# Performance work log

Measured on AMD Instinct MI355X. Metric: run time of the kernel, lower is better.

The kernel has to match this reference:

```python
import jax, jax.numpy as jnp
import numpy as np

SAMPLE_RATE = 44100.0


def _peaking_coeffs(freq, gain_db, q, fs):
    """RBJ cookbook peaking-EQ biquad coefficients (as in dasp-pytorch).
    freq/gain_db/q: [B, K]. Returns normalized b0,b1,b2,a1,a2 each [B, K]."""
    A = jnp.power(10.0, gain_db / 40.0)
    w0 = 2.0 * jnp.pi * freq / fs
    cosw = jnp.cos(w0)
    alpha = jnp.sin(w0) / (2.0 * q)
    b0 = 1.0 + alpha * A
    b1 = -2.0 * cosw
    b2 = 1.0 - alpha * A
    a0 = 1.0 + alpha / A
    a1 = -2.0 * cosw
    a2 = 1.0 - alpha / A
    inv_a0 = 1.0 / a0
    return b0 * inv_a0, b1 * inv_a0, b2 * inv_a0, a1 * inv_a0, a2 * inv_a0


def setup_inputs() -> dict:
    key = jax.random.key(0)
    k1, k2, k3, k4 = jax.random.split(key, 4)
    B, C, T, K = 32, 2, 262144, 6
    audio = jax.random.normal(k1, (B, C, T), dtype=jnp.float32) * 0.1
    # realistic EQ parameter ranges
    frequencies = 100.0 + jax.random.uniform(k2, (B, K), dtype=jnp.float32) * 9900.0  # 100 Hz .. 10 kHz
    gains = jax.random.normal(k3, (B, K), dtype=jnp.float32) * 6.0                     # ~ +/- 6 dB
    q_factors = 0.5 + jax.random.uniform(k4, (B, K), dtype=jnp.float32) * 3.0          # 0.5 .. 3.5
    return {"audio": audio, "frequencies": frequencies, "gains": gains, "q_factors": q_factors}


def reference(audio, frequencies, gains, q_factors):
    # audio: [B, C, T]; per-batch cascade of K peaking biquads over time.
    B, C, T = audio.shape
    K = frequencies.shape[1]
    b0, b1, b2, a1, a2 = _peaking_coeffs(frequencies, gains, q_factors, SAMPLE_RATE)
    # [K, B, 1] for broadcasting over channels
    b0, b1, b2, a1, a2 = (jnp.transpose(c)[:, :, None] for c in (b0, b1, b2, a1, a2))

    def step(carry, x):  # x: [B, C], one time sample through the whole cascade
        s1, s2 = carry  # each [K, B, C], direct-form II transposed states
        y = x
        ns1, ns2 = [], []
        for k in range(K):  # small fixed band loop (structurally sequential cascade)
            yk = b0[k] * y + s1[k]
            ns1.append(b1[k] * y - a1[k] * yk + s2[k])
            ns2.append(b2[k] * y - a2[k] * yk)
            y = yk
        return (jnp.stack(ns1), jnp.stack(ns2)), y

    init = (jnp.zeros((K, B, C), audio.dtype), jnp.zeros((K, B, C), audio.dtype))
    xs = jnp.moveaxis(audio, 2, 0)  # [T, B, C]
    _, ys = jax.lax.scan(step, init, xs)
    return jnp.moveaxis(ys, 0, 2)  # [B, C, T]
```

## Files before the change

### kernel.cpp

```cpp
#include <hip/hip_runtime.h>
#include <math.h>

namespace {
constexpr int B = 32, C = 2, T = 262144, K = 6;
constexpr int SEG = 1024;
constexpr int L = T / SEG;
constexpr int NBC = B * C;
constexpr int NST = 2 * K;
constexpr int LOG2L = 8;
constexpr int GP = SEG / 64;
constexpr int LOG2GP = 4;
constexpr int TS = 16;
constexpr int NT = L / TS;
constexpr int WPB = SEG / 64;
constexpr float FS = 44100.0f;
}

__device__ __forceinline__ float rl(float v, int lane) {
  return __int_as_float(__builtin_amdgcn_readlane(__float_as_int(v), lane));
}

__global__ void eq_coeffs(const float* __restrict__ fr, const float* __restrict__ gn,
                          const float* __restrict__ qf, float* __restrict__ cf) {
  int i = blockIdx.x * blockDim.x + threadIdx.x;
  if (i >= B * K) return;
  float f = fr[i], g = gn[i], Q = qf[i];
  float A  = powf(10.0f, g * (1.0f / 40.0f));
  float w0 = 6.283185307179586f * f / FS;
  float cw = cosf(w0);
  float al = sinf(w0) / (2.0f * Q);
  float b0 = 1.0f + al * A;
  float b1 = -2.0f * cw;
  float b2 = 1.0f - al * A;
  float a0 = 1.0f + al / A;
  float a2 = 1.0f - al / A;
  float ia = 1.0f / a0;
  float* p = cf + i * 5;
  p[0] = b0 * ia; p[1] = b1 * ia; p[2] = b2 * ia; p[3] = b1 * ia; p[4] = a2 * ia;
}

template <bool WRITE_OUT>
__global__ __launch_bounds__(64, 1) void eq_pass(const float* __restrict__ x,
                                                 const float* __restrict__ cf,
                                                 const float* __restrict__ st_in,
                                                 float* __restrict__ st_out,
                                                 float* __restrict__ y) {
  __shared__ float sIn[2][64][17];
  __shared__ float sOut[2][64][17];

  int l = threadIdx.x;
  int wid = blockIdx.x;
  int bc = wid / WPB;
  int segbase = (wid % WPB) * 64;
  int b = bc / C;
  int tid = bc * SEG + segbase + l;

  float b0[K], b1[K], b2[K], a1[K], a2[K];
#pragma unroll
  for (int k = 0; k < K; ++k) {
    const float* p = cf + (b * K + k) * 5;
    b0[k] = p[0]; b1[k] = p[1]; b2[k] = p[2]; a1[k] = p[3]; a2[k] = p[4];
  }

  float s1[K], s2[K];
  if (WRITE_OUT) {
    const float4* si = reinterpret_cast<const float4*>(st_in + (size_t)tid * NST);
    float4 v0 = si[0], v1 = si[1], v2 = si[2];
    s1[0] = v0.x; s2[0] = v0.y; s1[1] = v0.z; s2[1] = v0.w;
    s1[2] = v1.x; s2[2] = v1.y; s1[3] = v1.z; s2[3] = v1.w;
    s1[4] = v2.x; s2[4] = v2.y; s1[5] = v2.z; s2[5] = v2.w;
  } else {
#pragma unroll
    for (int k = 0; k < K; ++k) { s1[k] = 0.0f; s2[k] = 0.0f; }
  }

  const float4* xp4 = reinterpret_cast<const float4*>(x + (size_t)bc * T + (size_t)segbase * L);
  float4* yp4 = reinterpret_cast<float4*>(y + (size_t)bc * T + (size_t)segbase * L);
  constexpr int Q4 = L / 4;

  int sj = l >> 2;
  int qj = l & 3;

  float4 ra[4], rb[4];
#pragma unroll
  for (int j = 0; j < 4; ++j) ra[j] = xp4[(size_t)(j * 16 + sj) * Q4 + qj];
#pragma unroll
  for (int j = 0; j < 4; ++j) rb[j] = xp4[(size_t)(j * 16 + sj) * Q4 + 4 + qj];

  auto tile = [&](float4 (&r)[4], int t, int pb) {
#pragma unroll
    for (int j = 0; j < 4; ++j) {
      int seg = j * 16 + sj;
      sIn[pb][seg][qj * 4 + 0] = r[j].x;
      sIn[pb][seg][qj * 4 + 1] = r[j].y;
      sIn[pb][seg][qj * 4 + 2] = r[j].z;
      sIn[pb][seg][qj * 4 + 3] = r[j].w;
    }
    if (t + 2 < NT) {
#pragma unroll
      for (int j = 0; j < 4; ++j)
        r[j] = xp4[(size_t)(j * 16 + sj) * Q4 + (size_t)(t + 2) * 4 + qj];
    }
    float out16[TS];
#pragma unroll
    for (int i = 0; i < TS; ++i) {
      float yv = sIn[pb][l][i];
#pragma unroll
      for (int k = 0; k < K; ++k) {
        float yk = fmaf(b0[k], yv, s1[k]);
        float t1 = fmaf(b1[k], yv, s2[k]);
        s1[k] = fmaf(-a1[k], yk, t1);
        float t2 = b2[k] * yv;
        s2[k] = fmaf(-a2[k], yk, t2);
        yv = yk;
      }
      out16[i] = yv;
    }
    if (WRITE_OUT) {
#pragma unroll
      for (int i = 0; i < TS; ++i) sOut[pb][l][i] = out16[i];
#pragma unroll
      for (int j = 0; j < 4; ++j) {
        int seg = j * 16 + sj;
        float4 o;
        o.x = sOut[pb][seg][qj * 4 + 0];
        o.y = sOut[pb][seg][qj * 4 + 1];
        o.z = sOut[pb][seg][qj * 4 + 2];
        o.w = sOut[pb][seg][qj * 4 + 3];
        yp4[(size_t)seg * Q4 + (size_t)t * 4 + qj] = o;
      }
    }
  };

  for (int tt = 0; tt < NT; tt += 2) {
    tile(ra, tt, 0);
    tile(rb, tt + 1, 1);
  }

  if (!WRITE_OUT) {
    float4* so = reinterpret_cast<float4*>(st_out + (size_t)tid * NST);
    so[0] = make_float4(s1[0], s2[0], s1[1], s2[1]);
    so[1] = make_float4(s1[2], s2[2], s1[3], s2[3]);
    so[2] = make_float4(s1[4], s2[4], s1[5], s2[5]);
  }
}

__global__ __launch_bounds__(64, 1) void eq_scan(const float* __restrict__ cf,
                                                 const float* __restrict__ zsf,
                                                 float* __restrict__ sif) {
  __shared__ float PhiL[NST][NST];
  __shared__ float Mx[NST][NST + 1];
  __shared__ float W[64][NST + 1];
  __shared__ float SL[64][NST + 1];

  int bc = blockIdx.x;
  int b = bc / C;
  int l = threadIdx.x;
  bool act = (l < NST);

  float b0[K], b1[K], b2[K], a1[K], a2[K];
#pragma unroll
  for (int k = 0; k < K; ++k) {
    const float* p = cf + (b * K + k) * 5;
    b0[k] = p[0]; b1[k] = p[1]; b2[k] = p[2]; a1[k] = p[3]; a2[k] = p[4];
  }

  float col[NST];
  {
    float s1[K], s2[K];
#pragma unroll
    for (int k = 0; k < K; ++k) {
      s1[k] = (l == 2 * k) ? 1.0f : 0.0f;
      s2[k] = (l == 2 * k + 1) ? 1.0f : 0.0f;
    }
    float yv = 0.0f;
#pragma unroll
    for (int k = 0; k < K; ++k) {
      float yk = fmaf(b0[k], yv, s1[k]);
      float t1 = fmaf(b1[k], yv, s2[k]);
      float ns1 = fmaf(-a1[k], yk, t1);
      float ns2 = fmaf(-a2[k], yk, b2[k] * yv);
      s1[k] = ns1; s2[k] = ns2; yv = yk;
    }
#pragma unroll
    for (int k = 0; k < K; ++k) { col[2 * k] = s1[k]; col[2 * k + 1] = s2[k]; }
  }

  for (int p = 0; p < LOG2L; ++p) {
    float nc[NST];
#pragma unroll
    for (int r = 0; r < NST; ++r) nc[r] = 0.0f;
#pragma unroll
    for (int m = 0; m < NST; ++m) {
      float w = col[m];
#pragma unroll
      for (int r = 0; r < NST; ++r) nc[r] = fmaf(rl(col[r], m), w, nc[r]);
    }
#pragma unroll
    for (int r = 0; r < NST; ++r) col[r] = nc[r];
  }
  if (act) {
#pragma unroll
    for (int r = 0; r < NST; ++r) PhiL[r][l] = col[r];
  }
  __syncthreads();

  for (int p = 0; p < LOG2GP; ++p) {
    float nc[NST];
#pragma unroll
    for (int r = 0; r < NST; ++r) nc[r] = 0.0f;
#pragma unroll
    for (int m = 0; m < NST; ++m) {
      float w = col[m];
#pragma unroll
      for (int r = 0; r < NST; ++r) nc[r] = fmaf(rl(col[r], m), w, nc[r]);
    }
#pragma unroll
    for (int r = 0; r < NST; ++r) col[r] = nc[r];
  }
  if (act) {
#pragma unroll
    for (int r = 0; r < NST; ++r) Mx[r][l] = col[r];
  }
  __syncthreads();
  float row[NST];
#pragma unroll
  for (int m = 0; m < NST; ++m) row[m] = act ? Mx[l][m] : 0.0f;

  float phi[NST][NST];
#pragma unroll
  for (int r = 0; r < NST; ++r)
#pragma unroll
    for (int m = 0; m < NST; ++m) phi[r][m] = PhiL[r][m];

  const float* zb = zsf + ((size_t)bc * SEG + (size_t)l * GP) * NST;
  float s[NST];
#pragma unroll
  for (int r = 0; r < NST; ++r) s[r] = 0.0f;
  {
    float zc[NST], zn[NST];
    const float4* zp = reinterpret_cast<const float4*>(zb);
    float4 v0 = zp[0], v1 = zp[1], v2 = zp[2];
    zc[0] = v0.x; zc[1] = v0.y; zc[2] = v0.z; zc[3] = v0.w;
    zc[4] = v1.x; zc[5] = v1.y; zc[6] = v1.z; zc[7] = v1.w;
    zc[8] = v2.x; zc[9] = v2.y; zc[10] = v2.z; zc[11] = v2.w;
    for (int j = 0; j < GP; ++j) {
      if (j + 1 < GP) {
        const float4* zq = reinterpret_cast<const float4*>(zb + (size_t)(j + 1) * NST);
        float4 w0 = zq[0], w1 = zq[1], w2 = zq[2];
        zn[0] = w0.x; zn[1] = w0.y; zn[2] = w0.z; zn[3] = w0.w;
        zn[4] = w1.x; zn[5] = w1.y; zn[6] = w1.z; zn[7] = w1.w;
        zn[8] = w2.x; zn[9] = w2.y; zn[10] = w2.z; zn[11] = w2.w;
      }
      float ns[NST];
#pragma unroll
      for (int r = 0; r < NST; ++r) {
        float a = zc[r];
#pragma unroll
        for (int m = 0; m < NST; ++m) a = fmaf(phi[r][m], s[m], a);
        ns[r] = a;
      }
#pragma unroll
      for (int r = 0; r < NST; ++r) s[r] = ns[r];
#pragma unroll
      for (int r = 0; r < NST; ++r) zc[r] = zn[r];
    }
  }
#pragma unroll
  for (int r = 0; r < NST; ++r) W[l][r] = s[r];
  __syncthreads();

  {
    float sv = 0.0f;
    for (int i = 0; i < 64; ++i) {
      if (act) SL[i][l] = sv;
      float wv = act ? W[i][l] : 0.0f;
      float t0 = fmaf(row[0], rl(sv, 0), fmaf(row[1], rl(sv, 1), row[2] * rl(sv, 2)));
      float t1 = fmaf(row[3], rl(sv, 3), fmaf(row[4], rl(sv, 4), row[5] * rl(sv, 5)));
      float t2 = fmaf(row[6], rl(sv, 6), fmaf(row[7], rl(sv, 7), row[8] * rl(sv, 8)));
      float t3 = fmaf(row[9], rl(sv, 9), fmaf(row[10], rl(sv, 10), row[11] * rl(sv, 11)));
      sv = ((t0 + t1) + (t2 + t3)) + wv;
    }
  }
  __syncthreads();

  float sg[NST];
#pragma unroll
  for (int r = 0; r < NST; ++r) sg[r] = SL[l][r];
  {
    float zc[NST], zn[NST];
    const float4* zp = reinterpret_cast<const float4*>(zb);
    float4 v0 = zp[0], v1 = zp[1], v2 = zp[2];
    zc[0] = v0.x; zc[1] = v0.y; zc[2] = v0.z; zc[3] = v0.w;
    zc[4] = v1.x; zc[5] = v1.y; zc[6] = v1.z; zc[7] = v1.w;
    zc[8] = v2.x; zc[9] = v2.y; zc[10] = v2.z; zc[11] = v2.w;
    float* ob = sif + ((size_t)bc * SEG + (size_t)l * GP) * NST;
    for (int j = 0; j < GP; ++j) {
      if (j + 1 < GP) {
        const float4* zq = reinterpret_cast<const float4*>(zb + (size_t)(j + 1) * NST);
        float4 w0 = zq[0], w1 = zq[1], w2 = zq[2];
        zn[0] = w0.x; zn[1] = w0.y; zn[2] = w0.z; zn[3] = w0.w;
        zn[4] = w1.x; zn[5] = w1.y; zn[6] = w1.z; zn[7] = w1.w;
        zn[8] = w2.x; zn[9] = w2.y; zn[10] = w2.z; zn[11] = w2.w;
      }
      float4* op = reinterpret_cast<float4*>(ob + (size_t)j * NST);
      op[0] = make_float4(sg[0], sg[1], sg[2], sg[3]);
      op[1] = make_float4(sg[4], sg[5], sg[6], sg[7]);
      op[2] = make_float4(sg[8], sg[9], sg[10], sg[11]);
      float ns[NST];
#pragma unroll
      for (int r = 0; r < NST; ++r) {
        float a = zc[r];
#pragma unroll
        for (int m = 0; m < NST; ++m) a = fmaf(phi[r][m], sg[m], a);
        ns[r] = a;
      }
#pragma unroll
      for (int r = 0; r < NST; ++r) sg[r] = ns[r];
#pragma unroll
      for (int r = 0; r < NST; ++r) zc[r] = zn[r];
    }
  }
}

extern "C" void kernel_launch(void* const* d_in, const int* in_sizes, int n_in,
                              void* d_out, int out_size, void* d_ws, size_t ws_size,
                              hipStream_t stream) {
  const float* audio = (const float*)d_in[0];
  const float* fr    = (const float*)d_in[1];
  const float* gn    = (const float*)d_in[2];
  const float* qf    = (const float*)d_in[3];
  float* out = (float*)d_out;

  float* cf  = (float*)d_ws;
  float* zsf = cf + B * K * 5;
  float* sif = zsf + (size_t)NBC * SEG * NST;

  hipLaunchKernelGGL(eq_coeffs, dim3((B * K + 63) / 64), dim3(64), 0, stream,
                     fr, gn, qf, cf);
  hipLaunchKernelGGL((eq_pass<false>), dim3(NBC * WPB), dim3(64), 0, stream,
                     audio, cf, nullptr, zsf, out);
  hipLaunchKernelGGL(eq_scan, dim3(NBC), dim3(64), 0, stream, cf, zsf, sif);
  hipLaunchKernelGGL((eq_pass<true>), dim3(NBC * WPB), dim3(64), 0, stream,
                     audio, cf, sif, nullptr, out);
}
```

Baseline: 76.80 us.

## Double segment count, fold coefficient kernel into first pass, widen scan to four waves

Segments per channel are doubled so each thread filters half as many samples, and launch bounds allow two blocks per CU, giving more parallel work in both filtering passes. The separate coefficient kernel is removed: the first pass computes the biquad coefficients in-register and one block per batch writes them to the workspace for later kernels. The scan kernel uses 256 threads in a three-level hierarchy (per-thread groups of 8, per-wave serial scan, then cross-wave carry via precomputed matrix powers). This adds more state traffic and more scan work per channel in exchange for shorter serial chains and one fewer launch.

```diff
diff --git a/kernel.cpp b/kernel.cpp
--- a/kernel.cpp
+++ b/kernel.cpp
@@ -3,16 +3,16 @@
 
 namespace {
 constexpr int B = 32, C = 2, T = 262144, K = 6;
-constexpr int SEG = 1024;
+constexpr int SEG = 2048;
 constexpr int L = T / SEG;
 constexpr int NBC = B * C;
 constexpr int NST = 2 * K;
-constexpr int LOG2L = 8;
-constexpr int GP = SEG / 64;
-constexpr int LOG2GP = 4;
+constexpr int LOG2L = 7;
 constexpr int TS = 16;
 constexpr int NT = L / TS;
 constexpr int WPB = SEG / 64;
+constexpr int GP = 8;
+constexpr int NW = 4;
 constexpr float FS = 44100.0f;
 }
 
@@ -20,28 +20,63 @@
   return __int_as_float(__builtin_amdgcn_readlane(__float_as_int(v), lane));
 }
 
-__global__ void eq_coeffs(const float* __restrict__ fr, const float* __restrict__ gn,
-                          const float* __restrict__ qf, float* __restrict__ cf) {
-  int i = blockIdx.x * blockDim.x + threadIdx.x;
-  if (i >= B * K) return;
-  float f = fr[i], g = gn[i], Q = qf[i];
-  float A  = powf(10.0f, g * (1.0f / 40.0f));
-  float w0 = 6.283185307179586f * f / FS;
-  float cw = cosf(w0);
-  float al = sinf(w0) / (2.0f * Q);
-  float b0 = 1.0f + al * A;
-  float b1 = -2.0f * cw;
-  float b2 = 1.0f - al * A;
-  float a0 = 1.0f + al / A;
-  float a2 = 1.0f - al / A;
-  float ia = 1.0f / a0;
-  float* p = cf + i * 5;
-  p[0] = b0 * ia; p[1] = b1 * ia; p[2] = b2 * ia; p[3] = b1 * ia; p[4] = a2 * ia;
+__device__ __forceinline__ void ld12(const float* p, float (&v)[NST]) {
+  const float4* q = reinterpret_cast<const float4*>(p);
+  float4 a = q[0], b4 = q[1], c4 = q[2];
+  v[0] = a.x; v[1] = a.y; v[2] = a.z; v[3] = a.w;
+  v[4] = b4.x; v[5] = b4.y; v[6] = b4.z; v[7] = b4.w;
+  v[8] = c4.x; v[9] = c4.y; v[10] = c4.z; v[11] = c4.w;
+}
+
+__device__ __forceinline__ void st12(float* p, const float (&v)[NST]) {
+  float4* q = reinterpret_cast<float4*>(p);
+  q[0] = make_float4(v[0], v[1], v[2], v[3]);
+  q[1] = make_float4(v[4], v[5], v[6], v[7]);
+  q[2] = make_float4(v[8], v[9], v[10], v[11]);
+}
+
+__device__ __forceinline__ void affine(const float (&M)[NST][NST], float (&s)[NST],
+                                       const float (&z)[NST]) {
+  float ns[NST];
+#pragma unroll
+  for (int r = 0; r < NST; ++r) {
+    float a = z[r];
+#pragma unroll
+    for (int m = 0; m < NST; ++m) a = fmaf(M[r][m], s[m], a);
+    ns[r] = a;
+  }
+#pragma unroll
+  for (int r = 0; r < NST; ++r) s[r] = ns[r];
+}
+
+__device__ __forceinline__ void coeffs_for_b(const float* __restrict__ fr,
+                                             const float* __restrict__ gn,
+                                             const float* __restrict__ qf, int b,
+                                             float (&cb0)[K], float (&cb1)[K],
+                                             float (&cb2)[K], float (&ca1)[K],
+                                             float (&ca2)[K]) {
+#pragma unroll
+  for (int k = 0; k < K; ++k) {
+    float f = fr[b * K + k], g = gn[b * K + k], Q = qf[b * K + k];
+    float A  = powf(10.0f, g * (1.0f / 40.0f));
+    float w0 = 6.283185307179586f * f / FS;
+    float cw = cosf(w0);
+    float al = sinf(w0) / (2.0f * Q);
+    float ia = 1.0f / (1.0f + al / A);
+    cb0[k] = (1.0f + al * A) * ia;
+    cb1[k] = (-2.0f * cw) * ia;
+    cb2[k] = (1.0f - al * A) * ia;
+    ca1[k] = (-2.0f * cw) * ia;
+    ca2[k] = (1.0f - al / A) * ia;
+  }
 }
 
 template <bool WRITE_OUT>
-__global__ __launch_bounds__(64, 1) void eq_pass(const float* __restrict__ x,
-                                                 const float* __restrict__ cf,
+__global__ __launch_bounds__(64, 2) void eq_pass(const float* __restrict__ x,
+                                                 const float* __restrict__ fr,
+                                                 const float* __restrict__ gn,
+                                                 const float* __restrict__ qf,
+                                                 float* __restrict__ cf,
                                                  const float* __restrict__ st_in,
                                                  float* __restrict__ st_out,
                                                  float* __restrict__ y) {
@@ -55,25 +90,6 @@
   int b = bc / C;
   int tid = bc * SEG + segbase + l;
 
-  float b0[K], b1[K], b2[K], a1[K], a2[K];
-#pragma unroll
-  for (int k = 0; k < K; ++k) {
-    const float* p = cf + (b * K + k) * 5;
-    b0[k] = p[0]; b1[k] = p[1]; b2[k] = p[2]; a1[k] = p[3]; a2[k] = p[4];
-  }
-
-  float s1[K], s2[K];
-  if (WRITE_OUT) {
-    const float4* si = reinterpret_cast<const float4*>(st_in + (size_t)tid * NST);
-    float4 v0 = si[0], v1 = si[1], v2 = si[2];
-    s1[0] = v0.x; s2[0] = v0.y; s1[1] = v0.z; s2[1] = v0.w;
-    s1[2] = v1.x; s2[2] = v1.y; s1[3] = v1.z; s2[3] = v1.w;
-    s1[4] = v2.x; s2[4] = v2.y; s1[5] = v2.z; s2[5] = v2.w;
-  } else {
-#pragma unroll
-    for (int k = 0; k < K; ++k) { s1[k] = 0.0f; s2[k] = 0.0f; }
-  }
-
   const float4* xp4 = reinterpret_cast<const float4*>(x + (size_t)bc * T + (size_t)segbase * L);
   float4* yp4 = reinterpret_cast<float4*>(y + (size_t)bc * T + (size_t)segbase * L);
   constexpr int Q4 = L / 4;
@@ -86,6 +102,37 @@
   for (int j = 0; j < 4; ++j) ra[j] = xp4[(size_t)(j * 16 + sj) * Q4 + qj];
 #pragma unroll
   for (int j = 0; j < 4; ++j) rb[j] = xp4[(size_t)(j * 16 + sj) * Q4 + 4 + qj];
+
+  float b0[K], b1c[K], b2c[K], a1c[K], a2c[K];
+  if (!WRITE_OUT) {
+    coeffs_for_b(fr, gn, qf, b, b0, b1c, b2c, a1c, a2c);
+    if ((wid % (WPB * C)) == 0) {
+#pragma unroll
+      for (int k = 0; k < K; ++k) {
+        if (l == k) {
+          float* p = cf + (b * K + k) * 5;
+          p[0] = b0[k]; p[1] = b1c[k]; p[2] = b2c[k]; p[3] = a1c[k]; p[4] = a2c[k];
+        }
+      }
+    }
+  } else {
+#pragma unroll
+    for (int k = 0; k < K; ++k) {
+      const float* p = cf + (b * K + k) * 5;
+      b0[k] = p[0]; b1c[k] = p[1]; b2c[k] = p[2]; a1c[k] = p[3]; a2c[k] = p[4];
+    }
+  }
+
+  float s1[K], s2[K];
+  if (WRITE_OUT) {
+    float st[NST];
+    ld12(st_in + (size_t)tid * NST, st);
+#pragma unroll
+    for (int k = 0; k < K; ++k) { s1[k] = st[2 * k]; s2[k] = st[2 * k + 1]; }
+  } else {
+#pragma unroll
+    for (int k = 0; k < K; ++k) { s1[k] = 0.0f; s2[k] = 0.0f; }
+  }
 
   auto tile = [&](float4 (&r)[4], int t, int pb) {
 #pragma unroll
@@ -108,10 +155,10 @@
 #pragma unroll
       for (int k = 0; k < K; ++k) {
         float yk = fmaf(b0[k], yv, s1[k]);
-        float t1 = fmaf(b1[k], yv, s2[k]);
-        s1[k] = fmaf(-a1[k], yk, t1);
-        float t2 = b2[k] * yv;
-        s2[k] = fmaf(-a2[k], yk, t2);
+        float t1 = fmaf(b1c[k], yv, s2[k]);
+        s1[k] = fmaf(-a1c[k], yk, t1);
+        float t2 = b2c[k] * yv;
+        s2[k] = fmaf(-a2c[k], yk, t2);
         yv = yk;
       }
       out16[i] = yv;
@@ -138,31 +185,35 @@
   }
 
   if (!WRITE_OUT) {
-    float4* so = reinterpret_cast<float4*>(st_out + (size_t)tid * NST);
-    so[0] = make_float4(s1[0], s2[0], s1[1], s2[1]);
-    so[1] = make_float4(s1[2], s2[2], s1[3], s2[3]);
-    so[2] = make_float4(s1[4], s2[4], s1[5], s2[5]);
-  }
-}
-
-__global__ __launch_bounds__(64, 1) void eq_scan(const float* __restrict__ cf,
-                                                 const float* __restrict__ zsf,
-                                                 float* __restrict__ sif) {
+    float st[NST];
+#pragma unroll
+    for (int k = 0; k < K; ++k) { st[2 * k] = s1[k]; st[2 * k + 1] = s2[k]; }
+    st12(st_out + (size_t)tid * NST, st);
+  }
+}
+
+__global__ __launch_bounds__(256, 1) void eq_scan(const float* __restrict__ cf,
+                                                  const float* __restrict__ zsf,
+                                                  float* __restrict__ sif) {
   __shared__ float PhiL[NST][NST];
-  __shared__ float Mx[NST][NST + 1];
-  __shared__ float W[64][NST + 1];
-  __shared__ float SL[64][NST + 1];
+  __shared__ float Rg[NST][NST + 1];
+  __shared__ float Rw[NST][NST + 1];
+  __shared__ float FB[NW][64][NST + 1];
+  __shared__ float SL[NW][64][NST + 1];
+  __shared__ float WF[NW][NST + 1];
 
   int bc = blockIdx.x;
   int b = bc / C;
-  int l = threadIdx.x;
+  int t = threadIdx.x;
+  int w = t >> 6;
+  int l = t & 63;
   bool act = (l < NST);
 
-  float b0[K], b1[K], b2[K], a1[K], a2[K];
+  float b0[K], b1c[K], b2c[K], a1c[K], a2c[K];
 #pragma unroll
   for (int k = 0; k < K; ++k) {
     const float* p = cf + (b * K + k) * 5;
-    b0[k] = p[0]; b1[k] = p[1]; b2[k] = p[2]; a1[k] = p[3]; a2[k] = p[4];
+    b0[k] = p[0]; b1c[k] = p[1]; b2c[k] = p[2]; a1c[k] = p[3]; a2c[k] = p[4];
   }
 
   float col[NST];
@@ -177,148 +228,120 @@
 #pragma unroll
     for (int k = 0; k < K; ++k) {
       float yk = fmaf(b0[k], yv, s1[k]);
-      float t1 = fmaf(b1[k], yv, s2[k]);
-      float ns1 = fmaf(-a1[k], yk, t1);
-      float ns2 = fmaf(-a2[k], yk, b2[k] * yv);
+      float t1 = fmaf(b1c[k], yv, s2[k]);
+      float ns1 = fmaf(-a1c[k], yk, t1);
+      float ns2 = fmaf(-a2c[k], yk, b2c[k] * yv);
       s1[k] = ns1; s2[k] = ns2; yv = yk;
     }
 #pragma unroll
     for (int k = 0; k < K; ++k) { col[2 * k] = s1[k]; col[2 * k + 1] = s2[k]; }
   }
 
-  for (int p = 0; p < LOG2L; ++p) {
+  auto square = [&]() {
     float nc[NST];
 #pragma unroll
     for (int r = 0; r < NST; ++r) nc[r] = 0.0f;
 #pragma unroll
     for (int m = 0; m < NST; ++m) {
-      float w = col[m];
-#pragma unroll
-      for (int r = 0; r < NST; ++r) nc[r] = fmaf(rl(col[r], m), w, nc[r]);
+      float wv = col[m];
+#pragma unroll
+      for (int r = 0; r < NST; ++r) nc[r] = fmaf(rl(col[r], m), wv, nc[r]);
     }
 #pragma unroll
     for (int r = 0; r < NST; ++r) col[r] = nc[r];
-  }
-  if (act) {
+  };
+
+  for (int p = 0; p < LOG2L; ++p) square();
+  if (w == 0 && act) {
 #pragma unroll
     for (int r = 0; r < NST; ++r) PhiL[r][l] = col[r];
   }
+  for (int p = 0; p < 3; ++p) square();
+  if (w == 0 && act) {
+#pragma unroll
+    for (int r = 0; r < NST; ++r) Rg[r][l] = col[r];
+  }
+  for (int p = 0; p < 6; ++p) square();
+  if (w == 0 && act) {
+#pragma unroll
+    for (int r = 0; r < NST; ++r) Rw[r][l] = col[r];
+  }
   __syncthreads();
 
-  for (int p = 0; p < LOG2GP; ++p) {
-    float nc[NST];
-#pragma unroll
-    for (int r = 0; r < NST; ++r) nc[r] = 0.0f;
-#pragma unroll
-    for (int m = 0; m < NST; ++m) {
-      float w = col[m];
-#pragma unroll
-      for (int r = 0; r < NST; ++r) nc[r] = fmaf(rl(col[r], m), w, nc[r]);
-    }
-#pragma unroll
-    for (int r = 0; r < NST; ++r) col[r] = nc[r];
-  }
-  if (act) {
-#pragma unroll
-    for (int r = 0; r < NST; ++r) Mx[r][l] = col[r];
-  }
-  __syncthreads();
-  float row[NST];
-#pragma unroll
-  for (int m = 0; m < NST; ++m) row[m] = act ? Mx[l][m] : 0.0f;
-
+  float rowg[NST], roww[NST];
+#pragma unroll
+  for (int m = 0; m < NST; ++m) {
+    rowg[m] = act ? Rg[l][m] : 0.0f;
+    roww[m] = act ? Rw[l][m] : 0.0f;
+  }
   float phi[NST][NST];
 #pragma unroll
   for (int r = 0; r < NST; ++r)
 #pragma unroll
     for (int m = 0; m < NST; ++m) phi[r][m] = PhiL[r][m];
 
-  const float* zb = zsf + ((size_t)bc * SEG + (size_t)l * GP) * NST;
+  const float* zb = zsf + ((size_t)bc * SEG + (size_t)t * GP) * NST;
   float s[NST];
-#pragma unroll
-  for (int r = 0; r < NST; ++r) s[r] = 0.0f;
-  {
-    float zc[NST], zn[NST];
-    const float4* zp = reinterpret_cast<const float4*>(zb);
-    float4 v0 = zp[0], v1 = zp[1], v2 = zp[2];
-    zc[0] = v0.x; zc[1] = v0.y; zc[2] = v0.z; zc[3] = v0.w;
-    zc[4] = v1.x; zc[5] = v1.y; zc[6] = v1.z; zc[7] = v1.w;
-    zc[8] = v2.x; zc[9] = v2.y; zc[10] = v2.z; zc[11] = v2.w;
-    for (int j = 0; j < GP; ++j) {
-      if (j + 1 < GP) {
-        const float4* zq = reinterpret_cast<const float4*>(zb + (size_t)(j + 1) * NST);
-        float4 w0 = zq[0], w1 = zq[1], w2 = zq[2];
-        zn[0] = w0.x; zn[1] = w0.y; zn[2] = w0.z; zn[3] = w0.w;
-        zn[4] = w1.x; zn[5] = w1.y; zn[6] = w1.z; zn[7] = w1.w;
-        zn[8] = w2.x; zn[9] = w2.y; zn[10] = w2.z; zn[11] = w2.w;
-      }
-      float ns[NST];
-#pragma unroll
-      for (int r = 0; r < NST; ++r) {
-        float a = zc[r];
-#pragma unroll
-        for (int m = 0; m < NST; ++m) a = fmaf(phi[r][m], s[m], a);
-        ns[r] = a;
-      }
-#pragma unroll
-      for (int r = 0; r < NST; ++r) s[r] = ns[r];
-#pragma unroll
-      for (int r = 0; r < NST; ++r) zc[r] = zn[r];
-    }
-  }
-#pragma unroll
-  for (int r = 0; r < NST; ++r) W[l][r] = s[r];
+  ld12(zb, s);
+#pragma unroll
+  for (int j = 1; j < GP; ++j) {
+    float zc[NST];
+    ld12(zb + (size_t)j * NST, zc);
+    affine(phi, s, zc);
+  }
+#pragma unroll
+  for (int r = 0; r < NST; ++r) FB[w][l][r] = s[r];
   __syncthreads();
 
   {
     float sv = 0.0f;
     for (int i = 0; i < 64; ++i) {
-      if (act) SL[i][l] = sv;
-      float wv = act ? W[i][l] : 0.0f;
-      float t0 = fmaf(row[0], rl(sv, 0), fmaf(row[1], rl(sv, 1), row[2] * rl(sv, 2)));
-      float t1 = fmaf(row[3], rl(sv, 3), fmaf(row[4], rl(sv, 4), row[5] * rl(sv, 5)));
-      float t2 = fmaf(row[6], rl(sv, 6), fmaf(row[7], rl(sv, 7), row[8] * rl(sv, 8)));
-      float t3 = fmaf(row[9], rl(sv, 9), fmaf(row[10], rl(sv, 10), row[11] * rl(sv, 11)));
+      float wv = act ? FB[w][i][l] : 0.0f;
+      float t0 = fmaf(rowg[0], rl(sv, 0), fmaf(rowg[1], rl(sv, 1), rowg[2] * rl(sv, 2)));
+      float t1 = fmaf(rowg[3], rl(sv, 3), fmaf(rowg[4], rl(sv, 4), rowg[5] * rl(sv, 5)));
+      float t2 = fmaf(rowg[6], rl(sv, 6), fmaf(rowg[7], rl(sv, 7), rowg[8] * rl(sv, 8)));
+      float t3 = fmaf(rowg[9], rl(sv, 9), fmaf(rowg[10], rl(sv, 10), rowg[11] * rl(sv, 11)));
       sv = ((t0 + t1) + (t2 + t3)) + wv;
     }
+    if (act) WF[w][l] = sv;
   }
   __syncthreads();
 
+  float swv = 0.0f;
+  for (int w2 = 0; w2 < w; ++w2) {
+    float wfv = act ? WF[w2][l] : 0.0f;
+    float t0 = fmaf(roww[0], rl(swv, 0), fmaf(roww[1], rl(swv, 1), roww[2] * rl(swv, 2)));
+    float t1 = fmaf(roww[3], rl(swv, 3), fmaf(roww[4], rl(swv, 4), roww[5] * rl(swv, 5)));
+    float t2 = fmaf(roww[6], rl(swv, 6), fmaf(roww[7], rl(swv, 7), roww[8] * rl(swv, 8)));
+    float t3 = fmaf(roww[9], rl(swv, 9), fmaf(roww[10], rl(swv, 10), roww[11] * rl(swv, 11)));
+    swv = ((t0 + t1) + (t2 + t3)) + wfv;
+  }
+
+  {
+    float sv = swv;
+    for (int i = 0; i < 64; ++i) {
+      if (act) SL[w][i][l] = sv;
+      float wv = act ? FB[w][i][l] : 0.0f;
+      float t0 = fmaf(rowg[0], rl(sv, 0), fmaf(rowg[1], rl(sv, 1), rowg[2] * rl(sv, 2)));
+      float t1 = fmaf(rowg[3], rl(sv, 3), fmaf(rowg[4], rl(sv, 4), rowg[5] * rl(sv, 5)));
+      float t2 = fmaf(rowg[6], rl(sv, 6), fmaf(rowg[7], rl(sv, 7), rowg[8] * rl(sv, 8)));
+      float t3 = fmaf(rowg[9], rl(sv, 9), fmaf(rowg[10], rl(sv, 10), rowg[11] * rl(sv, 11)));
+      sv = ((t0 + t1) + (t2 + t3)) + wv;
+    }
+  }
+  __syncthreads();
+
   float sg[NST];
 #pragma unroll
-  for (int r = 0; r < NST; ++r) sg[r] = SL[l][r];
-  {
-    float zc[NST], zn[NST];
-    const float4* zp = reinterpret_cast<const float4*>(zb);
-    float4 v0 = zp[0], v1 = zp[1], v2 = zp[2];
-    zc[0] = v0.x; zc[1] = v0.y; zc[2] = v0.z; zc[3] = v0.w;
-    zc[4] = v1.x; zc[5] = v1.y; zc[6] = v1.z; zc[7] = v1.w;
-    zc[8] = v2.x; zc[9] = v2.y; zc[10] = v2.z; zc[11] = v2.w;
-    float* ob = sif + ((size_t)bc * SEG + (size_t)l * GP) * NST;
-    for (int j = 0; j < GP; ++j) {
-      if (j + 1 < GP) {
-        const float4* zq = reinterpret_cast<const float4*>(zb + (size_t)(j + 1) * NST);
-        float4 w0 = zq[0], w1 = zq[1], w2 = zq[2];
-        zn[0] = w0.x; zn[1] = w0.y; zn[2] = w0.z; zn[3] = w0.w;
-        zn[4] = w1.x; zn[5] = w1.y; zn[6] = w1.z; zn[7] = w1.w;
-        zn[8] = w2.x; zn[9] = w2.y; zn[10] = w2.z; zn[11] = w2.w;
-      }
-      float4* op = reinterpret_cast<float4*>(ob + (size_t)j * NST);
-      op[0] = make_float4(sg[0], sg[1], sg[2], sg[3]);
-      op[1] = make_float4(sg[4], sg[5], sg[6], sg[7]);
-      op[2] = make_float4(sg[8], sg[9], sg[10], sg[11]);
-      float ns[NST];
-#pragma unroll
-      for (int r = 0; r < NST; ++r) {
-        float a = zc[r];
-#pragma unroll
-        for (int m = 0; m < NST; ++m) a = fmaf(phi[r][m], sg[m], a);
-        ns[r] = a;
-      }
-#pragma unroll
-      for (int r = 0; r < NST; ++r) sg[r] = ns[r];
-#pragma unroll
-      for (int r = 0; r < NST; ++r) zc[r] = zn[r];
+  for (int r = 0; r < NST; ++r) sg[r] = SL[w][l][r];
+  float* ob = sif + ((size_t)bc * SEG + (size_t)t * GP) * NST;
+#pragma unroll
+  for (int j = 0; j < GP; ++j) {
+    st12(ob + (size_t)j * NST, sg);
+    if (j + 1 < GP) {
+      float zc[NST];
+      ld12(zb + (size_t)j * NST, zc);
+      affine(phi, sg, zc);
     }
   }
 }
@@ -336,11 +359,9 @@
   float* zsf = cf + B * K * 5;
   float* sif = zsf + (size_t)NBC * SEG * NST;
 
-  hipLaunchKernelGGL(eq_coeffs, dim3((B * K + 63) / 64), dim3(64), 0, stream,
-                     fr, gn, qf, cf);
   hipLaunchKernelGGL((eq_pass<false>), dim3(NBC * WPB), dim3(64), 0, stream,
-                     audio, cf, nullptr, zsf, out);
-  hipLaunchKernelGGL(eq_scan, dim3(NBC), dim3(64), 0, stream, cf, zsf, sif);
+                     audio, fr, gn, qf, cf, nullptr, zsf, out);
+  hipLaunchKernelGGL(eq_scan, dim3(NBC), dim3(256), 0, stream, cf, zsf, sif);
   hipLaunchKernelGGL((eq_pass<true>), dim3(NBC * WPB), dim3(64), 0, stream,
-                     audio, cf, sif, nullptr, out);
-}
+                     audio, fr, gn, qf, cf, sif, nullptr, out);
+}
```

Result: slower. 84.44 us (+9.9%).
